# Optimization experiments

Measured on AMD Instinct MI355X. Metric: run time of the kernel, lower is better.

The kernel has to match this reference:

```python
import itertools
import jax, jax.numpy as jnp
import numpy as np

B = 2
D = H = W = 64          # volume size
F_IN = 8                # input features
F_OUT = 8               # output features
TRF_MULT = 1.0


def setup_inputs() -> dict:
    key = jax.random.key(0)
    k1, k2, k3, k4 = jax.random.split(key, 4)
    x = jax.random.normal(k1, (B, D, H, W, F_IN), dtype=jnp.float32)
    # mult init: RandomNormal(mean=1/F_IN, stddev=0.01)
    mult = 1.0 / F_IN + 0.01 * jax.random.normal(k2, (D, H, W, F_IN, F_OUT), dtype=jnp.float32)
    # trf init: RandomNormal(mean=0, stddev=0.001)
    trf = 0.001 * jax.random.normal(k3, (D, H, W, F_IN, F_OUT, 3), dtype=jnp.float32)
    # bias init: RandomNormal(mean=1/F_IN, stddev=0.01)
    bias = 1.0 / F_IN + 0.01 * jax.random.normal(k4, (D, H, W, F_OUT), dtype=jnp.float32)
    return {"x": x, "mult": mult, "trf": trf, "bias": bias}


def _forward(x, mult, trf, bias):
    dims = (D, H, W)
    grid = jnp.stack(
        jnp.meshgrid(*[jnp.arange(d, dtype=jnp.float32) for d in dims], indexing='ij'), -1
    )  # [D,H,W,3]
    # per-voxel, per-(i,j) sampling location = identity grid + displacement
    loc = grid[:, :, :, None, None, :] + trf * TRF_MULT          # [D,H,W,Fi,Fo,3]
    max_f = jnp.array([d - 1 for d in dims], dtype=jnp.float32)
    max_i = jnp.array([d - 1 for d in dims], dtype=jnp.int32)
    cl = jnp.clip(loc, 0.0, max_f)                               # clipped continuous loc
    l0 = jnp.clip(jnp.floor(loc), 0.0, max_f).astype(jnp.int32)  # lower corner
    l1 = jnp.clip(l0 + 1, 0, max_i)                              # upper corner
    d1 = l1.astype(jnp.float32) - cl  # weight for corner bit 0 (neurite convention)
    d0 = 1.0 - d1                     # weight for corner bit 1
    ich = jnp.arange(F_IN)[None, None, None, :, None]  # channel index, broadcasts to [D,H,W,Fi,Fo]

    def warp_all_pairs(vol):  # vol [D,H,W,F_IN] -> sampled [D,H,W,Fi,Fo]
        out = jnp.zeros((D, H, W, F_IN, F_OUT), dtype=vol.dtype)
        for c in itertools.product((0, 1), repeat=3):  # 8 trilinear corners
            i0 = (l1 if c[0] else l0)[..., 0]
            i1 = (l1 if c[1] else l0)[..., 1]
            i2 = (l1 if c[2] else l0)[..., 2]
            w = ((d0[..., 0] if c[0] else d1[..., 0])
                 * (d0[..., 1] if c[1] else d1[..., 1])
                 * (d0[..., 2] if c[2] else d1[..., 2]))
            out = out + w * vol[i0, i1, i2, ich]
        return out

    def per_batch(vol):
        sampled = warp_all_pairs(vol)                        # [D,H,W,Fi,Fo]
        y = jnp.einsum('dhwij,dhwij->dhwj', sampled, mult)   # local linear combine
        # NB: source adds bias inside the loop over input features -> F_IN copies
        return y + F_IN * bias

    return jax.vmap(per_batch)(x)


def reference(x, mult, trf, bias):
    return _forward(x, mult, trf, bias)
```

## Files before the change

kernel.cpp:

```cpp
#include <hip/hip_runtime.h>


#define BATCH_STRIDE 2097152

__global__ __launch_bounds__(512) void lclt_kernel(
    const float* __restrict__ x,
    const float* __restrict__ mult,
    const float* __restrict__ trf,
    const float* __restrict__ bias,
    float* __restrict__ out)
{
    __shared__ float sx[4 * 4 * 4 * 16];
    __shared__ float strf[8 * 192];

    const int tid  = threadIdx.x;
    const int wv   = tid >> 6;
    const int lane = tid & 63;
    const int i    = lane >> 3;

    const int bt  = blockIdx.x;
    const int tzb = (bt >> 10) << 1;
    const int tyb = ((bt >> 5) & 31) << 1;
    const int txb = (bt & 31) << 1;

    #pragma unroll
    for (int s = 0; s < 2; ++s) {
        const int sidx = tid + s * 512;
        const int b   = sidx >> 9;
        const int rem = sidx & 511;
        const int ic  = rem & 7;
        const int hx  = (rem >> 3) & 3;
        const int hy  = (rem >> 5) & 3;
        const int hz  = rem >> 7;
        const int gz = min(max(tzb - 1 + hz, 0), 63);
        const int gy = min(max(tyb - 1 + hy, 0), 63);
        const int gx = min(max(txb - 1 + hx, 0), 63);
        const float val = x[b * BATCH_STRIDE + (gz << 15) + (gy << 9) + (gx << 3) + ic];
        const int hv = ((hz << 2) + hy) * 4 + hx;
        sx[(hv << 4) + (ic << 1) + b] = val;
    }

    const int lz = wv >> 2, ly = (wv >> 1) & 1, lx = wv & 1;
    const int vz = tzb + lz, vy = tyb + ly, vx = txb + lx;
    const int v  = (vz << 12) + (vy << 6) + vx;

    const float* tb = trf + (size_t)v * 192;
    {
        const float t0 = tb[lane];
        const float t1 = tb[lane + 64];
        const float t2 = tb[lane + 128];
        float* sw = strf + wv * 192;
        sw[lane]       = t0;
        sw[lane + 64]  = t1;
        sw[lane + 128] = t2;
    }

    const float m = mult[(size_t)v * 64 + lane];

    __syncthreads();

    const float* sw = strf + wv * 192 + lane * 3;
    const float tz = sw[0];
    const float ty = sw[1];
    const float tx = sw[2];

    const float locz = (float)vz + tz;
    const float locy = (float)vy + ty;
    const float locx = (float)vx + tx;

    const float clz = fminf(fmaxf(locz, 0.0f), 63.0f);
    const float cly = fminf(fmaxf(locy, 0.0f), 63.0f);
    const float clx = fminf(fmaxf(locx, 0.0f), 63.0f);

    const int z0 = (int)fminf(fmaxf(floorf(locz), 0.0f), 63.0f);
    const int y0 = (int)fminf(fmaxf(floorf(locy), 0.0f), 63.0f);
    const int x0 = (int)fminf(fmaxf(floorf(locx), 0.0f), 63.0f);
    const int z1 = min(z0 + 1, 63);
    const int y1 = min(y0 + 1, 63);
    const int x1 = min(x0 + 1, 63);

    const float d1z = (float)z1 - clz, d0z = 1.0f - d1z;
    const float d1y = (float)y1 - cly, d0y = 1.0f - d1y;
    const float d1x = (float)x1 - clx, d0x = 1.0f - d1x;

    const float wzy00 = d1z * d1y, wzy01 = d1z * d0y;
    const float wzy10 = d0z * d1y, wzy11 = d0z * d0y;
    const float w000 = wzy00 * d1x, w001 = wzy00 * d0x;
    const float w010 = wzy01 * d1x, w011 = wzy01 * d0x;
    const float w100 = wzy10 * d1x, w101 = wzy10 * d0x;
    const float w110 = wzy11 * d1x, w111 = wzy11 * d0x;

    const int hz0 = z0 - tzb + 1, hz1 = z1 - tzb + 1;
    const int hy0 = y0 - tyb + 1, hy1 = y1 - tyb + 1;
    const int hx0 = x0 - txb + 1, hx1 = x1 - txb + 1;

    const float2* sx2 = (const float2*)sx;
    const int r00 = ((hz0 << 2) + hy0) << 2;
    const int r01 = ((hz0 << 2) + hy1) << 2;
    const int r10 = ((hz1 << 2) + hy0) << 2;
    const int r11 = ((hz1 << 2) + hy1) << 2;

    const float2 g000 = sx2[((r00 + hx0) << 3) + i];
    const float2 g001 = sx2[((r00 + hx1) << 3) + i];
    const float2 g010 = sx2[((r01 + hx0) << 3) + i];
    const float2 g011 = sx2[((r01 + hx1) << 3) + i];
    const float2 g100 = sx2[((r10 + hx0) << 3) + i];
    const float2 g101 = sx2[((r10 + hx1) << 3) + i];
    const float2 g110 = sx2[((r11 + hx0) << 3) + i];
    const float2 g111 = sx2[((r11 + hx1) << 3) + i];

    float s0 = w000 * g000.x + w001 * g001.x + w010 * g010.x + w011 * g011.x
             + w100 * g100.x + w101 * g101.x + w110 * g110.x + w111 * g111.x;
    float s1 = w000 * g000.y + w001 * g001.y + w010 * g010.y + w011 * g011.y
             + w100 * g100.y + w101 * g101.y + w110 * g110.y + w111 * g111.y;

    float acc0 = m * s0;
    float acc1 = m * s1;

    acc0 += __shfl_xor(acc0, 8);
    acc1 += __shfl_xor(acc1, 8);
    acc0 += __shfl_xor(acc0, 16);
    acc1 += __shfl_xor(acc1, 16);
    acc0 += __shfl_xor(acc0, 32);
    acc1 += __shfl_xor(acc1, 32);

    if (lane < 16) {
        const int j = lane & 7;
        const float bv = bias[v * 8 + j];
        const float r = ((lane < 8) ? acc0 : acc1) + 8.0f * bv;
        out[((lane < 8) ? 0 : BATCH_STRIDE) + v * 8 + j] = r;
    }
}

extern "C" void kernel_launch(void* const* d_in, const int* in_sizes, int n_in,
                              void* d_out, int out_size, void* d_ws, size_t ws_size,
                              hipStream_t stream) {
    const float* x    = (const float*)d_in[0];
    const float* mult = (const float*)d_in[1];
    const float* trf  = (const float*)d_in[2];
    const float* bias = (const float*)d_in[3];
    float* out = (float*)d_out;

    lclt_kernel<<<32768, 512, 0, stream>>>(x, mult, trf, bias, out);
}
```

Baseline: 340.8 us.

## Process four x-voxels per wave with wider halo tile and nontemporal loads

Each block now covers a 4x2x2 voxel tile with 4 waves, and each wave loops over 4 consecutive x voxels. The halo tile becomes 6x4x4, so less halo is reloaded per output voxel. The trf and mult loads become 16-byte nontemporal vector loads, and outputs use nontemporal stores. The trade is fewer waves in flight per block and a serial loop per wave in exchange for better halo reuse and wider memory transactions.

```diff
diff --git a/kernel.cpp b/kernel.cpp
--- a/kernel.cpp
+++ b/kernel.cpp
@@ -3,15 +3,17 @@
 
 #define BATCH_STRIDE 2097152
 
-__global__ __launch_bounds__(512) void lclt_kernel(
+typedef float vf4 __attribute__((ext_vector_type(4)));
+
+__global__ __launch_bounds__(256) void lclt_kernel(
     const float* __restrict__ x,
     const float* __restrict__ mult,
     const float* __restrict__ trf,
     const float* __restrict__ bias,
     float* __restrict__ out)
 {
-    __shared__ float sx[4 * 4 * 4 * 16];
-    __shared__ float strf[8 * 192];
+    __shared__ float sx[4 * 4 * 6 * 8 * 2];
+    __shared__ float strf[4 * 4 * 192];
 
     const int tid  = threadIdx.x;
     const int wv   = tid >> 6;
@@ -19,116 +21,128 @@
     const int i    = lane >> 3;
 
     const int bt  = blockIdx.x;
-    const int tzb = (bt >> 10) << 1;
-    const int tyb = ((bt >> 5) & 31) << 1;
-    const int txb = (bt & 31) << 1;
+    const int txb = (bt & 15) << 2;
+    const int tyb = ((bt >> 4) & 31) << 1;
+    const int tzb = (bt >> 9) << 1;
 
     #pragma unroll
-    for (int s = 0; s < 2; ++s) {
-        const int sidx = tid + s * 512;
-        const int b   = sidx >> 9;
-        const int rem = sidx & 511;
-        const int ic  = rem & 7;
-        const int hx  = (rem >> 3) & 3;
-        const int hy  = (rem >> 5) & 3;
-        const int hz  = rem >> 7;
+    for (int s = 0; s < 6; ++s) {
+        const int sidx = tid + (s << 8);
+        const int b    = sidx >= 768;
+        const int rem  = sidx - (b ? 768 : 0);
+        const int ic   = rem & 7;
+        const int t48  = rem / 48;
+        const int hx   = (rem >> 3) - t48 * 6;
+        const int hy   = t48 & 3;
+        const int hz   = t48 >> 2;
         const int gz = min(max(tzb - 1 + hz, 0), 63);
         const int gy = min(max(tyb - 1 + hy, 0), 63);
         const int gx = min(max(txb - 1 + hx, 0), 63);
         const float val = x[b * BATCH_STRIDE + (gz << 15) + (gy << 9) + (gx << 3) + ic];
-        const int hv = ((hz << 2) + hy) * 4 + hx;
-        sx[(hv << 4) + (ic << 1) + b] = val;
+        sx[((((hz << 2) + hy) * 6 + hx) << 4) + (ic << 1) + b] = val;
     }
 
-    const int lz = wv >> 2, ly = (wv >> 1) & 1, lx = wv & 1;
-    const int vz = tzb + lz, vy = tyb + ly, vx = txb + lx;
-    const int v  = (vz << 12) + (vy << 6) + vx;
+    const int vz = tzb + (wv >> 1);
+    const int vy = tyb + (wv & 1);
+    const int vzy = (vz << 12) + (vy << 6);
 
-    const float* tb = trf + (size_t)v * 192;
-    {
-        const float t0 = tb[lane];
-        const float t1 = tb[lane + 64];
-        const float t2 = tb[lane + 128];
-        float* sw = strf + wv * 192;
-        sw[lane]       = t0;
-        sw[lane + 64]  = t1;
-        sw[lane + 128] = t2;
+    float* swt = strf + wv * 768;
+    if (lane < 48) {
+        #pragma unroll
+        for (int k = 0; k < 4; ++k) {
+            const vf4* tp = (const vf4*)(trf + (size_t)(vzy + txb + k) * 192);
+            const vf4 t = __builtin_nontemporal_load(tp + lane);
+            ((vf4*)(swt + k * 192))[lane] = t;
+        }
     }
 
-    const float m = mult[(size_t)v * 64 + lane];
+    float mreg[4], breg[4];
+    #pragma unroll
+    for (int k = 0; k < 4; ++k) {
+        const int v = vzy + txb + k;
+        mreg[k] = __builtin_nontemporal_load(mult + (size_t)v * 64 + lane);
+        breg[k] = __builtin_nontemporal_load(bias + (size_t)v * 8 + (lane & 7));
+    }
 
     __syncthreads();
 
-    const float* sw = strf + wv * 192 + lane * 3;
-    const float tz = sw[0];
-    const float ty = sw[1];
-    const float tx = sw[2];
+    const float2* sx2 = (const float2*)sx;
 
-    const float locz = (float)vz + tz;
-    const float locy = (float)vy + ty;
-    const float locx = (float)vx + tx;
+    #pragma unroll
+    for (int k = 0; k < 4; ++k) {
+        const int vx = txb + k;
+        const int v  = vzy + vx;
 
-    const float clz = fminf(fmaxf(locz, 0.0f), 63.0f);
-    const float cly = fminf(fmaxf(locy, 0.0f), 63.0f);
-    const float clx = fminf(fmaxf(locx, 0.0f), 63.0f);
+        const float* sw = swt + k * 192 + lane * 3;
+        const float tz = sw[0];
+        const float ty = sw[1];
+        const float tx = sw[2];
 
-    const int z0 = (int)fminf(fmaxf(floorf(locz), 0.0f), 63.0f);
-    const int y0 = (int)fminf(fmaxf(floorf(locy), 0.0f), 63.0f);
-    const int x0 = (int)fminf(fmaxf(floorf(locx), 0.0f), 63.0f);
-    const int z1 = min(z0 + 1, 63);
-    const int y1 = min(y0 + 1, 63);
-    const int x1 = min(x0 + 1, 63);
+        const float locz = (float)vz + tz;
+        const float locy = (float)vy + ty;
+        const float locx = (float)vx + tx;
 
-    const float d1z = (float)z1 - clz, d0z = 1.0f - d1z;
-    const float d1y = (float)y1 - cly, d0y = 1.0f - d1y;
-    const float d1x = (float)x1 - clx, d0x = 1.0f - d1x;
+        const float clz = fminf(fmaxf(locz, 0.0f), 63.0f);
+        const float cly = fminf(fmaxf(locy, 0.0f), 63.0f);
+        const float clx = fminf(fmaxf(locx, 0.0f), 63.0f);
 
-    const float wzy00 = d1z * d1y, wzy01 = d1z * d0y;
-    const float wzy10 = d0z * d1y, wzy11 = d0z * d0y;
-    const float w000 = wzy00 * d1x, w001 = wzy00 * d0x;
-    const float w010 = wzy01 * d1x, w011 = wzy01 * d0x;
-    const float w100 = wzy10 * d1x, w101 = wzy10 * d0x;
-    const float w110 = wzy11 * d1x, w111 = wzy11 * d0x;
+        const int z0 = (int)fminf(fmaxf(floorf(locz), 0.0f), 63.0f);
+        const int y0 = (int)fminf(fmaxf(floorf(locy), 0.0f), 63.0f);
+        const int x0 = (int)fminf(fmaxf(floorf(locx), 0.0f), 63.0f);
+        const int z1 = min(z0 + 1, 63);
+        const int y1 = min(y0 + 1, 63);
+        const int x1 = min(x0 + 1, 63);
 
-    const int hz0 = z0 - tzb + 1, hz1 = z1 - tzb + 1;
-    const int hy0 = y0 - tyb + 1, hy1 = y1 - tyb + 1;
-    const int hx0 = x0 - txb + 1, hx1 = x1 - txb + 1;
+        const float d1z = (float)z1 - clz, d0z = 1.0f - d1z;
+        const float d1y = (float)y1 - cly, d0y = 1.0f - d1y;
+        const float d1x = (float)x1 - clx, d0x = 1.0f - d1x;
 
-    const float2* sx2 = (const float2*)sx;
-    const int r00 = ((hz0 << 2) + hy0) << 2;
-    const int r01 = ((hz0 << 2) + hy1) << 2;
-    const int r10 = ((hz1 << 2) + hy0) << 2;
-    const int r11 = ((hz1 << 2) + hy1) << 2;
+        const float wzy00 = d1z * d1y, wzy01 = d1z * d0y;
+        const float wzy10 = d0z * d1y, wzy11 = d0z * d0y;
+        const float w000 = wzy00 * d1x, w001 = wzy00 * d0x;
+        const float w010 = wzy01 * d1x, w011 = wzy01 * d0x;
+        const float w100 = wzy10 * d1x, w101 = wzy10 * d0x;
+        const float w110 = wzy11 * d1x, w111 = wzy11 * d0x;
 
-    const float2 g000 = sx2[((r00 + hx0) << 3) + i];
-    const float2 g001 = sx2[((r00 + hx1) << 3) + i];
-    const float2 g010 = sx2[((r01 + hx0) << 3) + i];
-    const float2 g011 = sx2[((r01 + hx1) << 3) + i];
-    const float2 g100 = sx2[((r10 + hx0) << 3) + i];
-    const float2 g101 = sx2[((r10 + hx1) << 3) + i];
-    const float2 g110 = sx2[((r11 + hx0) << 3) + i];
-    const float2 g111 = sx2[((r11 + hx1) << 3) + i];
+        const int hz0 = z0 - tzb + 1, hz1 = z1 - tzb + 1;
+        const int hy0 = y0 - tyb + 1, hy1 = y1 - tyb + 1;
+        const int hx0 = x0 - txb + 1, hx1 = x1 - txb + 1;
 
-    float s0 = w000 * g000.x + w001 * g001.x + w010 * g010.x + w011 * g011.x
-             + w100 * g100.x + w101 * g101.x + w110 * g110.x + w111 * g111.x;
-    float s1 = w000 * g000.y + w001 * g001.y + w010 * g010.y + w011 * g011.y
-             + w100 * g100.y + w101 * g101.y + w110 * g110.y + w111 * g111.y;
+        const int r00 = ((hz0 << 2) + hy0) * 6;
+        const int r01 = ((hz0 << 2) + hy1) * 6;
+        const int r10 = ((hz1 << 2) + hy0) * 6;
+        const int r11 = ((hz1 << 2) + hy1) * 6;
 
-    float acc0 = m * s0;
-    float acc1 = m * s1;
+        const float2 g000 = sx2[((r00 + hx0) << 3) + i];
+        const float2 g001 = sx2[((r00 + hx1) << 3) + i];
+        const float2 g010 = sx2[((r01 + hx0) << 3) + i];
+        const float2 g011 = sx2[((r01 + hx1) << 3) + i];
+        const float2 g100 = sx2[((r10 + hx0) << 3) + i];
+        const float2 g101 = sx2[((r10 + hx1) << 3) + i];
+        const float2 g110 = sx2[((r11 + hx0) << 3) + i];
+        const float2 g111 = sx2[((r11 + hx1) << 3) + i];
 
-    acc0 += __shfl_xor(acc0, 8);
-    acc1 += __shfl_xor(acc1, 8);
-    acc0 += __shfl_xor(acc0, 16);
-    acc1 += __shfl_xor(acc1, 16);
-    acc0 += __shfl_xor(acc0, 32);
-    acc1 += __shfl_xor(acc1, 32);
+        float s0 = w000 * g000.x + w001 * g001.x + w010 * g010.x + w011 * g011.x
+                 + w100 * g100.x + w101 * g101.x + w110 * g110.x + w111 * g111.x;
+        float s1 = w000 * g000.y + w001 * g001.y + w010 * g010.y + w011 * g011.y
+                 + w100 * g100.y + w101 * g101.y + w110 * g110.y + w111 * g111.y;
 
-    if (lane < 16) {
-        const int j = lane & 7;
-        const float bv = bias[v * 8 + j];
-        const float r = ((lane < 8) ? acc0 : acc1) + 8.0f * bv;
-        out[((lane < 8) ? 0 : BATCH_STRIDE) + v * 8 + j] = r;
+        float acc0 = mreg[k] * s0;
+        float acc1 = mreg[k] * s1;
+
+        acc0 += __shfl_xor(acc0, 8);
+        acc1 += __shfl_xor(acc1, 8);
+        acc0 += __shfl_xor(acc0, 16);
+        acc1 += __shfl_xor(acc1, 16);
+        acc0 += __shfl_xor(acc0, 32);
+        acc1 += __shfl_xor(acc1, 32);
+
+        if (lane < 16) {
+            const int j = lane & 7;
+            const float r = ((lane < 8) ? acc0 : acc1) + 8.0f * breg[k];
+            __builtin_nontemporal_store(
+                r, out + ((lane < 8) ? 0 : BATCH_STRIDE) + (size_t)v * 8 + j);
+        }
     }
 }
 
@@ -141,5 +155,5 @@
     const float* bias = (const float*)d_in[3];
     float* out = (float*)d_out;
 
-    lclt_kernel<<<32768, 512, 0, stream>>>(x, mult, trf, bias, out);
+    lclt_kernel<<<16384, 256, 0, stream>>>(x, mult, trf, bias, out);
 }
```

Result: faster. 331.5 us (-2.7%).
